# Performance work log

Measured on AMD Instinct MI355X. Metric: run time of the kernel, lower is better.

The kernel has to match this reference:

```python
import jax, jax.numpy as jnp
import numpy as np

B, S, E, KD = 4, 2048, 1024, 1024

def setup_inputs() -> dict:
    key = jax.random.key(0)
    k1, k2, k3, k4 = jax.random.split(key, 4)
    # nn.Linear weights are [out_features, in_features]
    x = jax.random.normal(k1, (B, S, E), dtype=jnp.float32)
    W_q = jax.random.normal(k2, (KD, E), dtype=jnp.float32) * (E ** -0.5)
    W_k = jax.random.normal(k3, (KD, E), dtype=jnp.float32) * (E ** -0.5)
    W_v = jax.random.normal(k4, (E, E), dtype=jnp.float32) * (E ** -0.5)
    return {"x": x, "W_q": W_q, "W_k": W_k, "W_v": W_v}

def reference(x, W_q, W_k, W_v):
    # Projections: y = x @ W.T  (torch Linear convention)
    Q = jnp.einsum('bse,ke->bsk', x, W_q)   # [B,S,KD]
    K = jnp.einsum('bse,ke->bsk', x, W_k)   # [B,S,KD]
    V = jnp.einsum('bse,fe->bsf', x, W_v)   # [B,S,E]
    key_dim = W_q.shape[0]
    scores = jnp.einsum('bqk,bsk->bqs', Q, K) / jnp.sqrt(jnp.asarray(key_dim, x.dtype))
    S_len = x.shape[1]
    causal = jnp.tril(jnp.ones((S_len, S_len), dtype=bool))  # [S,S]
    scores = jnp.where(causal, scores, -jnp.inf)
    weights = jax.nn.softmax(scores, axis=-1)                # [B,S,S]
    out = jnp.einsum('bqs,bsf->bqf', weights, V)             # [B,S,E]
    return out
```

## Files before the change

### kernel.cpp

```cpp
#include <hip/hip_runtime.h>

typedef _Float16 f16;
typedef _Float16 f16x8 __attribute__((ext_vector_type(8)));
typedef float    f32x4 __attribute__((ext_vector_type(4)));

__device__ __forceinline__ void gld_lds16(const void* g, void* l) {
    __builtin_amdgcn_global_load_lds((__attribute__((address_space(1))) void*)g,
                                     (__attribute__((address_space(3))) void*)l,
                                     16, 0, 0);
}

#define BARRIER() do { asm volatile("" ::: "memory"); \
                       __builtin_amdgcn_s_barrier();  \
                       asm volatile("" ::: "memory"); } while (0)

template<bool STG, int VM1, int VM4>
__device__ __forceinline__ void tile256(
    f32x4 (&acc)[8][4],
    const f16* Ak0, const f16* Ak1, const f16* Bk0, const f16* Bk1,
    const f16* gAn, const f16* gBn,
    f16* lAn, f16* lBn,
    int lda, int ldb)
{
    {
        f16x8 a[4], b[4];
        #pragma unroll
        for (int mf = 0; mf < 4; mf++) a[mf] = *(const f16x8*)(Ak0 + mf * 1024);
        #pragma unroll
        for (int nf = 0; nf < 4; nf++) b[nf] = *(const f16x8*)(Bk0 + nf * 1024);
        if (STG) {
            gld_lds16(gBn,                  lBn);
            gld_lds16(gBn + (long)64 * ldb, lBn + 4096);
        }
        BARRIER();
        __builtin_amdgcn_s_setprio(1);
        #pragma unroll
        for (int mf = 0; mf < 4; mf++)
            #pragma unroll
            for (int nf = 0; nf < 4; nf++)
                acc[mf][nf] = __builtin_amdgcn_mfma_f32_16x16x32_f16(
                    a[mf], b[nf], acc[mf][nf], 0, 0, 0);
        __builtin_amdgcn_s_setprio(0);
        if (VM1 == 2)      asm volatile("s_waitcnt vmcnt(2)" ::: "memory");
        else if (VM1 == 0) asm volatile("s_waitcnt vmcnt(0)" ::: "memory");
        BARRIER();
        f16x8 a2[4];
        #pragma unroll
        for (int mf = 0; mf < 4; mf++) a2[mf] = *(const f16x8*)(Ak0 + (mf + 4) * 1024);
        if (STG) {
            gld_lds16(gBn + (long)128 * ldb, lBn + 8192);
            gld_lds16(gBn + (long)192 * ldb, lBn + 12288);
        }
        BARRIER();
        __builtin_amdgcn_s_setprio(1);
        #pragma unroll
        for (int mf = 0; mf < 4; mf++)
            #pragma unroll
            for (int nf = 0; nf < 4; nf++)
                acc[mf + 4][nf] = __builtin_amdgcn_mfma_f32_16x16x32_f16(
                    a2[mf], b[nf], acc[mf + 4][nf], 0, 0, 0);
        __builtin_amdgcn_s_setprio(0);
        BARRIER();
    }
    {
        f16x8 a[4], b[4];
        #pragma unroll
        for (int mf = 0; mf < 4; mf++) a[mf] = *(const f16x8*)(Ak1 + mf * 1024);
        #pragma unroll
        for (int nf = 0; nf < 4; nf++) b[nf] = *(const f16x8*)(Bk1 + nf * 1024);
        if (STG) {
            gld_lds16(gAn,                   lAn);
            gld_lds16(gAn + (long)128 * lda, lAn + 8192);
        }
        BARRIER();
        __builtin_amdgcn_s_setprio(1);
        #pragma unroll
        for (int mf = 0; mf < 4; mf++)
            #pragma unroll
            for (int nf = 0; nf < 4; nf++)
                acc[mf][nf] = __builtin_amdgcn_mfma_f32_16x16x32_f16(
                    a[mf], b[nf], acc[mf][nf], 0, 0, 0);
        __builtin_amdgcn_s_setprio(0);
        BARRIER();
        f16x8 a2[4];
        #pragma unroll
        for (int mf = 0; mf < 4; mf++) a2[mf] = *(const f16x8*)(Ak1 + (mf + 4) * 1024);
        if (STG) {
            gld_lds16(gAn + (long)64 * lda,  lAn + 4096);
            gld_lds16(gAn + (long)192 * lda, lAn + 12288);
        }
        BARRIER();
        __builtin_amdgcn_s_setprio(1);
        #pragma unroll
        for (int mf = 0; mf < 4; mf++)
            #pragma unroll
            for (int nf = 0; nf < 4; nf++)
                acc[mf + 4][nf] = __builtin_amdgcn_mfma_f32_16x16x32_f16(
                    a2[mf], b[nf], acc[mf + 4][nf], 0, 0, 0);
        __builtin_amdgcn_s_setprio(0);
        if (VM4 == 2)      asm volatile("s_waitcnt vmcnt(2)" ::: "memory");
        else if (VM4 == 0) asm volatile("s_waitcnt vmcnt(0)" ::: "memory");
        BARRIER();
    }
}

__global__ void __launch_bounds__(512, 2)
gemm256_k1024(const f16* __restrict__ A, const f16* __restrict__ B,
              f16* __restrict__ C, int lda, int ldb, int ldc)
{
    const int m  = (int)blockIdx.x;
    const int L  = (m & 7) * 32 + (m >> 3);
    const int i0 = (L >> 3) * 256;
    const int j0 = (L & 7) * 256;

    __shared__ f16 Lds[2 * 32768] __attribute__((aligned(16)));

    const int tid  = threadIdx.x;
    const int lane = tid & 63;
    const int wave = tid >> 6;
    const int wm = wave >> 2, wn = wave & 3;
    const int row16 = lane & 15, quad = lane >> 4;
    const int swz = row16 & 7;

    const int c0 = (quad ^ swz) * 8;
    const int c1 = ((quad + 4) ^ swz) * 8;
    const f16* A0k0 = Lds + (wm * 128 + row16) * 64 + c0;
    const f16* A0k1 = Lds + (wm * 128 + row16) * 64 + c1;
    const f16* B0k0 = Lds + 16384 + (wn * 64 + row16) * 64 + c0;
    const f16* B0k1 = Lds + 16384 + (wn * 64 + row16) * 64 + c1;

    const int srow = tid >> 3;
    const int scol = ((tid & 7) ^ (srow & 7)) * 8;
    const f16* gA = A + (long)(i0 + srow) * lda + scol;
    const f16* gB = B + (long)(j0 + srow) * ldb + scol;
    f16* lA0 = Lds + tid * 8;
    f16* lB0 = Lds + 16384 + tid * 8;
    f16* lA1 = Lds + 32768 + tid * 8;
    f16* lB1 = Lds + 32768 + 16384 + tid * 8;

    gld_lds16(gB,                   lB0);
    gld_lds16(gB + (long)64 * ldb,  lB0 + 4096);
    gld_lds16(gB + (long)128 * ldb, lB0 + 8192);
    gld_lds16(gB + (long)192 * ldb, lB0 + 12288);
    gld_lds16(gA,                   lA0);
    gld_lds16(gA + (long)128 * lda, lA0 + 8192);
    gld_lds16(gA + (long)64 * lda,  lA0 + 4096);
    gld_lds16(gA + (long)192 * lda, lA0 + 12288);

    f32x4 acc[8][4] = {};

    asm volatile("s_waitcnt vmcnt(2)" ::: "memory");
    BARRIER();

    for (int t = 0; t < 14; t += 2) {
        tile256<true, 2, 2>(acc, A0k0, A0k1, B0k0, B0k1,
                            gA + (t + 1) * 64, gB + (t + 1) * 64,
                            lA1, lB1, lda, ldb);
        tile256<true, 2, 2>(acc, A0k0 + 32768, A0k1 + 32768,
                            B0k0 + 32768, B0k1 + 32768,
                            gA + (t + 2) * 64, gB + (t + 2) * 64,
                            lA0, lB0, lda, ldb);
    }
    tile256<true, 2, 2>(acc, A0k0, A0k1, B0k0, B0k1,
                        gA + 15 * 64, gB + 15 * 64, lA1, lB1, lda, ldb);
    tile256<false, 0, -1>(acc, A0k0 + 32768, A0k1 + 32768,
                          B0k0 + 32768, B0k1 + 32768,
                          nullptr, nullptr, nullptr, nullptr, lda, ldb);

    #pragma unroll
    for (int mf = 0; mf < 8; mf++) {
        const int r0 = i0 + wm * 128 + mf * 16 + quad * 4;
        #pragma unroll
        for (int nf = 0; nf < 4; nf++) {
            const int c = j0 + wn * 64 + nf * 16 + row16;
            #pragma unroll
            for (int r = 0; r < 4; r++)
                C[(long)(r0 + r) * ldc + c] = (f16)acc[mf][nf][r];
        }
    }
}

template<typename OutT>
__device__ __forceinline__ void gemm128_body(
    const f16* __restrict__ A, const f16* __restrict__ B, OutT* __restrict__ C,
    int lda, int ldb, int ldc, int Keff, float scale, int i0, int j0)
{
    __shared__ f16 As[128 * 64] __attribute__((aligned(16)));
    __shared__ f16 Bs[64 * 64]  __attribute__((aligned(16)));

    const int tid  = threadIdx.x;
    const int lane = tid & 63;
    const int wave = tid >> 6;
    const int row16 = lane & 15;
    const int quad  = lane >> 4;
    const int swz   = row16 & 7;
    const int wr = (wave >> 1) * 64;
    const int wc = (wave & 1) * 32;

    const int srow = tid >> 3;
    const int scol = ((tid & 7) ^ (srow & 7)) * 8;
    const f16* gA = A + (long)(i0 + srow) * lda + scol;
    const f16* gB = B + (long)(j0 + srow) * ldb + scol;
    f16* lA = As + tid * 8;
    f16* lB = Bs + tid * 8;

    f32x4 acc[4][2] = {};

    for (int k0 = 0; k0 < Keff; k0 += 64) {
        gld_lds16(gA + k0,                  lA);
        gld_lds16(gA + k0 + (long)32 * lda, lA + 32 * 64);
        gld_lds16(gA + k0 + (long)64 * lda, lA + 64 * 64);
        gld_lds16(gA + k0 + (long)96 * lda, lA + 96 * 64);
        gld_lds16(gB + k0,                  lB);
        gld_lds16(gB + k0 + (long)32 * ldb, lB + 32 * 64);
        __syncthreads();

        #pragma unroll
        for (int kk = 0; kk < 2; kk++) {
            f16x8 af[4], bf[2];
            #pragma unroll
            for (int t = 0; t < 4; t++)
                af[t] = *(const f16x8*)(As + (wr + t * 16 + row16) * 64
                                           + (((kk * 4 + quad) ^ swz) * 8));
            #pragma unroll
            for (int t = 0; t < 2; t++)
                bf[t] = *(const f16x8*)(Bs + (wc + t * 16 + row16) * 64
                                           + (((kk * 4 + quad) ^ swz) * 8));
            #pragma unroll
            for (int mt = 0; mt < 4; mt++)
                #pragma unroll
                for (int nt = 0; nt < 2; nt++)
                    acc[mt][nt] = __builtin_amdgcn_mfma_f32_16x16x32_f16(
                        af[mt], bf[nt], acc[mt][nt], 0, 0, 0);
        }
        __syncthreads();
    }

    #pragma unroll
    for (int mt = 0; mt < 4; mt++) {
        const int r0 = i0 + wr + mt * 16 + quad * 4;
        #pragma unroll
        for (int nt = 0; nt < 2; nt++) {
            const int c = j0 + wc + nt * 16 + row16;
            #pragma unroll
            for (int r = 0; r < 4; r++)
                C[(long)(r0 + r) * ldc + c] = (OutT)(acc[mt][nt][r] * scale);
        }
    }
}

__global__ void __launch_bounds__(256)
gemm_vt_sc(const f16* __restrict__ xh, const f16* __restrict__ wvh,
           const f16* __restrict__ QKh, f16* __restrict__ Vt,
           f16* __restrict__ Sc)
{
    const int blk = (int)blockIdx.x;
    if (blk < 1024) {
        const int L = (blk & 7) * 128 + (blk >> 3);
        const int j = L >> 3;
        const int i = L & 7;
        gemm128_body<f16>(wvh, xh, Vt, 1024, 1024, 8192, 1024, 1.f,
                          i * 128, j * 64);
    } else {
        const int m = blk - 1024;
        const int L = (m & 7) * 136 + (m >> 3);
        const int z = L / 272;
        const int r = L - z * 272;
        int y = 0;
        while ((y + 1) * (y + 2) <= r) y++;
        const int x = r - y * (y + 1);
        const long off = (long)z * (2048L * 2048);
        gemm128_body<f16>(QKh + off, QKh + 1024 + off, Sc + off,
                          2048, 2048, 2048, 1024, 0.03125f, y * 128, x * 64);
    }
}

__global__ void __launch_bounds__(256)
gemm_pv(const f16* __restrict__ Sc, const f16* __restrict__ Vt,
        float* __restrict__ out)
{
    const int z = (int)blockIdx.z;
    const int by = (int)gridDim.y - 1 - (int)blockIdx.y;
    const int i0 = by * 128;
    const int j0 = (int)blockIdx.x * 64;
    const int Keff = i0 + 128;
    gemm128_body<float>(Sc + (long)z * (2048L * 2048),
                        Vt + (long)z * 2048,
                        out + (long)z * (2048L * 1024),
                        2048, 8192, 1024, Keff, 1.f, i0, j0);
}

__global__ void __launch_bounds__(256)
softmax_causal(f16* __restrict__ Sc)
{
    const int S = 2048;
    const long rowg = blockIdx.x;
    const long b = rowg >> 11;
    const int  i = (int)(rowg & 2047);
    f16* row = Sc + ((b * S + i) * (long)S);
    const int L = ((i >> 7) + 1) << 7;

    const int tid = threadIdx.x;
    const int c0  = tid * 8;
    const int lane = tid & 63, wave = tid >> 6;
    const bool act = c0 < L;

    float v[8];
    float m = -3.4e38f;
    if (act) {
        f16x8 in = *(const f16x8*)(row + c0);
        #pragma unroll
        for (int j = 0; j < 8; j++) {
            const bool ok = (c0 + j) <= i;
            v[j] = ok ? (float)in[j] : -3.4e38f;
            m = fmaxf(m, v[j]);
        }
    }
    #pragma unroll
    for (int off = 32; off > 0; off >>= 1)
        m = fmaxf(m, __shfl_down(m, off, 64));
    __shared__ float redm[4];
    if (lane == 0) redm[wave] = m;
    __syncthreads();
    const float m0 = fmaxf(fmaxf(redm[0], redm[1]), fmaxf(redm[2], redm[3]));

    float e[8];
    float s = 0.f;
    if (act) {
        #pragma unroll
        for (int j = 0; j < 8; j++) {
            const bool ok = (c0 + j) <= i;
            e[j] = ok ? __expf(v[j] - m0) : 0.f;
            s += e[j];
        }
    }
    #pragma unroll
    for (int off = 32; off > 0; off >>= 1)
        s += __shfl_down(s, off, 64);
    __shared__ float reds[4];
    if (lane == 0) reds[wave] = s;
    __syncthreads();
    const float inv = 1.f / (reds[0] + reds[1] + reds[2] + reds[3]);

    if (act) {
        f16x8 o;
        #pragma unroll
        for (int j = 0; j < 8; j++) o[j] = (f16)(e[j] * inv);
        *(f16x8*)(row + c0) = o;
    }
}

__global__ void __launch_bounds__(256)
convert_all(const float* __restrict__ x, const float* __restrict__ Wq,
            const float* __restrict__ Wk, const float* __restrict__ Wv,
            f16* __restrict__ xh, f16* __restrict__ wh)
{
    const long blk = blockIdx.x;
    const float* src;
    f16* dst;
    long base;
    if (blk < 4096)      { src = x;  dst = xh;                    base = blk * 2048; }
    else if (blk < 4608) { src = Wq; dst = wh;                    base = (blk - 4096) * 2048; }
    else if (blk < 5120) { src = Wk; dst = wh + 1024L * 1024;     base = (blk - 4608) * 2048; }
    else                 { src = Wv; dst = wh + 2L * 1024 * 1024; base = (blk - 5120) * 2048; }
    const long i = base + (long)threadIdx.x * 8;
    f32x4 a = *(const f32x4*)(src + i);
    f32x4 b = *(const f32x4*)(src + i + 4);
    f16x8 o;
    o[0] = (f16)a[0]; o[1] = (f16)a[1]; o[2] = (f16)a[2]; o[3] = (f16)a[3];
    o[4] = (f16)b[0]; o[5] = (f16)b[1]; o[6] = (f16)b[2]; o[7] = (f16)b[3];
    *(f16x8*)(dst + i) = o;
}

extern "C" void kernel_launch(void* const* d_in, const int* in_sizes, int n_in,
                              void* d_out, int out_size, void* d_ws, size_t ws_size,
                              hipStream_t stream)
{
    (void)in_sizes; (void)n_in; (void)out_size; (void)ws_size;
    const float* x  = (const float*)d_in[0];
    const float* Wq = (const float*)d_in[1];
    const float* Wk = (const float*)d_in[2];
    const float* Wv = (const float*)d_in[3];
    float* out = (float*)d_out;

    const long NX = 4L * 2048 * 1024;
    const long NW = 1024L * 1024;

    char* p = (char*)d_ws;
    f16* xh  = (f16*)p; p += NX * 2;
    f16* wh  = (f16*)p; p += 3 * NW * 2;
    f16* QKh = (f16*)p; p += 2 * NX * 2;
    f16* Vt  = (f16*)p; p += NX * 2;
    f16* Sc  = (f16*)p; p += 4L * 2048 * 2048 * 2;
    f16* wvh = wh + 2L * NW;

    convert_all<<<5632, 256, 0, stream>>>(x, Wq, Wk, Wv, xh, wh);

    gemm256_k1024<<<256, 512, 0, stream>>>(
        xh, wh, QKh, 1024, 1024, 2048);

    gemm_vt_sc<<<2112, 256, 0, stream>>>(xh, wvh, QKh, Vt, Sc);

    softmax_causal<<<4 * 2048, 256, 0, stream>>>(Sc);

    gemm_pv<<<dim3(16, 16, 4), 256, 0, stream>>>(Sc, Vt, out);
}
```

Measured before the change: 227.4 us.

## Split-K the causal PV GEMM into balanced 512-wide chunks with atomic accumulation

The PV GEMM launch changes from a 2D grid of row/column tiles, whose causal K lengths vary a lot, to a flat grid of 2560 blocks. Each block handles at most a 512-wide slice of K for one output tile and adds its partial result into the fp32 output with atomicAdd. This is meant to even out per-block work and raise occupancy for the triangular workload. The cost is extra atomic traffic, and the output must already be zeroed before accumulation; no zeroing step is visible in this change.

```diff
diff --git a/kernel.cpp b/kernel.cpp
--- a/kernel.cpp
+++ b/kernel.cpp
@@ -180,10 +180,10 @@
     }
 }
 
-template<typename OutT>
+template<typename OutT, bool ATOMIC>
 __device__ __forceinline__ void gemm128_body(
     const f16* __restrict__ A, const f16* __restrict__ B, OutT* __restrict__ C,
-    int lda, int ldb, int ldc, int Keff, float scale, int i0, int j0)
+    int lda, int ldb, int ldc, int kLo, int kHi, float scale, int i0, int j0)
 {
     __shared__ f16 As[128 * 64] __attribute__((aligned(16)));
     __shared__ f16 Bs[64 * 64]  __attribute__((aligned(16)));
@@ -206,7 +206,7 @@
 
     f32x4 acc[4][2] = {};
 
-    for (int k0 = 0; k0 < Keff; k0 += 64) {
+    for (int k0 = kLo; k0 < kHi; k0 += 64) {
         gld_lds16(gA + k0,                  lA);
         gld_lds16(gA + k0 + (long)32 * lda, lA + 32 * 64);
         gld_lds16(gA + k0 + (long)64 * lda, lA + 64 * 64);
@@ -243,8 +243,13 @@
         for (int nt = 0; nt < 2; nt++) {
             const int c = j0 + wc + nt * 16 + row16;
             #pragma unroll
-            for (int r = 0; r < 4; r++)
-                C[(long)(r0 + r) * ldc + c] = (OutT)(acc[mt][nt][r] * scale);
+            for (int r = 0; r < 4; r++) {
+                if (ATOMIC)
+                    atomicAdd((float*)&C[(long)(r0 + r) * ldc + c],
+                              acc[mt][nt][r] * scale);
+                else
+                    C[(long)(r0 + r) * ldc + c] = (OutT)(acc[mt][nt][r] * scale);
+            }
         }
     }
 }
@@ -259,8 +264,8 @@
         const int L = (blk & 7) * 128 + (blk >> 3);
         const int j = L >> 3;
         const int i = L & 7;
-        gemm128_body<f16>(wvh, xh, Vt, 1024, 1024, 8192, 1024, 1.f,
-                          i * 128, j * 64);
+        gemm128_body<f16, false>(wvh, xh, Vt, 1024, 1024, 8192, 0, 1024, 1.f,
+                                 i * 128, j * 64);
     } else {
         const int m = blk - 1024;
         const int L = (m & 7) * 136 + (m >> 3);
@@ -270,8 +275,9 @@
         while ((y + 1) * (y + 2) <= r) y++;
         const int x = r - y * (y + 1);
         const long off = (long)z * (2048L * 2048);
-        gemm128_body<f16>(QKh + off, QKh + 1024 + off, Sc + off,
-                          2048, 2048, 2048, 1024, 0.03125f, y * 128, x * 64);
+        gemm128_body<f16, false>(QKh + off, QKh + 1024 + off, Sc + off,
+                                 2048, 2048, 2048, 0, 1024, 0.03125f,
+                                 y * 128, x * 64);
     }
 }
 
@@ -279,15 +285,28 @@
 gemm_pv(const f16* __restrict__ Sc, const f16* __restrict__ Vt,
         float* __restrict__ out)
 {
-    const int z = (int)blockIdx.z;
-    const int by = (int)gridDim.y - 1 - (int)blockIdx.y;
+    const int n = (int)blockIdx.x;
+    const int z = n / 640;
+    const int r = n - z * 640;
+    const int x = r / 40;
+    const int q = 39 - (r - x * 40);
+    int by = 0, cum = 0;
+    for (;;) {
+        const int nc = (by >> 2) + 1;
+        if (cum + nc > q) break;
+        cum += nc;
+        by++;
+    }
+    const int c = q - cum;
     const int i0 = by * 128;
-    const int j0 = (int)blockIdx.x * 64;
+    const int j0 = x * 64;
     const int Keff = i0 + 128;
-    gemm128_body<float>(Sc + (long)z * (2048L * 2048),
-                        Vt + (long)z * 2048,
-                        out + (long)z * (2048L * 1024),
-                        2048, 8192, 1024, Keff, 1.f, i0, j0);
+    const int kLo = c * 512;
+    const int kHi = min(Keff, kLo + 512);
+    gemm128_body<float, true>(Sc + (long)z * (2048L * 2048),
+                              Vt + (long)z * 2048,
+                              out + (long)z * (2048L * 1024),
+                              2048, 8192, 1024, kLo, kHi, 1.f, i0, j0);
 }
 
 __global__ void __launch_bounds__(256)
@@ -403,5 +422,5 @@
 
     softmax_causal<<<4 * 2048, 256, 0, stream>>>(Sc);
 
-    gemm_pv<<<dim3(16, 16, 4), 256, 0, stream>>>(Sc, Vt, out);
-}
+    gemm_pv<<<2560, 256, 0, stream>>>(Sc, Vt, out);
+}
```

After: 246.8 us. 8.5% more time.
